# Performance work log

Hardware: AMD Instinct MI355X
Metric: run time of the kernel (lower is better)

The kernel has to match this reference:

```python
import jax, jax.numpy as jnp
import numpy as np

NUM_EMBEDDINGS = 8192
EMBEDDING_DIM = 256


def setup_inputs() -> dict:
    key = jax.random.key(0)
    k1, k2 = jax.random.split(key)
    z = jax.random.normal(k1, (16, EMBEDDING_DIM, 32, 32), dtype=jnp.float32)
    # nn.Embedding default init: N(0, 1)
    emb_table = jax.random.normal(k2, (NUM_EMBEDDINGS, EMBEDDING_DIM), dtype=jnp.float32)
    return {"z": z, "emb_table": emb_table}


def reference(z, emb_table):
    # z: [B, D, H, W]; emb_table: [K, D]
    B, D, H, W = z.shape
    # flatten to per-token vectors: [B*H*W, D]
    zf = z.reshape(B, D, H * W).transpose(0, 2, 1).reshape(B * H * W, D)
    Wt = jax.lax.stop_gradient(emb_table)  # original detaches W for distance
    # argmin of mean squared distance == argmin of squared distance;
    # expand ||z - w||^2 = ||z||^2 - 2 z.w + ||w||^2 (avoid (N,K,D) expansion)
    z_sq = jnp.sum(zf * zf, axis=-1, keepdims=True)          # [N, 1]
    w_sq = jnp.sum(Wt * Wt, axis=-1)                          # [K]
    dists = z_sq - 2.0 * (zf @ Wt.T) + w_sq                   # [N, K]
    token_ids = jnp.argmin(dists, axis=-1)                    # [N]
    quantized = emb_table[token_ids]                          # [N, D] (differentiable gather)
    return quantized.reshape(B, H * W, D).transpose(0, 2, 1).reshape(B, D, H, W)
```

## Files before the change

### kernel.cpp

```cpp
#include <hip/hip_runtime.h>
#include <stdint.h>

#define DIM 256
#define NEMB 8192
#define NTOK 16384
#define HW 1024

typedef __attribute__((ext_vector_type(4))) int int4v;

__device__ __forceinline__ void async_cp16(void* lds, const void* g) {
  __builtin_amdgcn_global_load_lds(
      (const __attribute__((address_space(1))) unsigned int*)g,
      (__attribute__((address_space(3))) unsigned int*)lds, 16, 0, 0);
}
__device__ __forceinline__ int q0_of(float x) {
  int q = __float2int_rn(x * 20.0f);
  return q > 127 ? 127 : (q < -127 ? -127 : q);
}
__device__ __forceinline__ int q1_of(float x, int q0) {
  float e = x * 20.0f - (float)q0;
  int q = __float2int_rn(e * 128.0f);
  return q > 127 ? 127 : (q < -127 ? -127 : q);
}
__device__ __forceinline__ unsigned int pack4(int a, int b, int c, int d) {
  return (unsigned int)(a & 0xff) | ((unsigned int)(b & 0xff) << 8) |
         ((unsigned int)(c & 0xff) << 16) | ((unsigned int)(d & 0xff) << 24);
}
__device__ __forceinline__ unsigned int med3u(unsigned int a, unsigned int b,
                                              unsigned int c) {
  unsigned int m;
  asm("v_med3_u32 %0, %1, %2, %3" : "=v"(m) : "v"(a), "v"(b), "v"(c));
  return m;
}
__device__ __forceinline__ void top3_insert(unsigned int v, unsigned int& m1,
                                            unsigned int& m2, unsigned int& m3) {
  unsigned int t2 = med3u(v, m1, m2);
  unsigned int t3 = med3u(v, m2, m3);
  m1 = v < m1 ? v : m1;
  m2 = t2;
  m3 = t3;
}

__global__ __launch_bounds__(256) void prep_kernel(
    const float* __restrict__ emb, unsigned int* __restrict__ q0w,
    unsigned int* __restrict__ q1w, int* __restrict__ iwsq2,
    const float* __restrict__ z, unsigned int* __restrict__ q0z) {
  __shared__ float tile[64][65];
  int tid = threadIdx.x;
  int lane = tid & 63;
  if (blockIdx.x < 2048) {
    int row = blockIdx.x * 4 + (tid >> 6);
    const float4 v = *(const float4*)(emb + (size_t)row * DIM + lane * 4);
    float s = v.x * v.x + v.y * v.y + v.z * v.z + v.w * v.w;
    int a0 = q0_of(v.x), b0 = q0_of(v.y), c0 = q0_of(v.z), d0 = q0_of(v.w);
    q0w[row * (DIM / 4) + lane] = pack4(a0, b0, c0, d0);
    q1w[row * (DIM / 4) + lane] =
        pack4(q1_of(v.x, a0), q1_of(v.y, b0), q1_of(v.z, c0), q1_of(v.w, d0));
#pragma unroll
    for (int off = 32; off > 0; off >>= 1) s += __shfl_xor(s, off, 64);
    if (lane == 0) iwsq2[row] = (int)rintf(s * 25600.0f) + 8192;
    return;
  }
  int idx = blockIdx.x - 2048;
  int b = idx >> 6, d0 = ((idx >> 4) & 3) * 64, hw0 = (idx & 15) * 64;
  int grp = tid >> 6;
  const float* src = z + (size_t)b * DIM * HW + hw0 + lane;
#pragma unroll
  for (int i = 0; i < 16; i++) {
    int dl = grp + i * 4;
    tile[dl][lane] = src[(size_t)(d0 + dl) * HW];
  }
  __syncthreads();
  int dq = tid & 15;
#pragma unroll
  for (int p = 0; p < 4; p++) {
    int n = (tid >> 4) + p * 16;
    int a0 = q0_of(tile[dq * 4 + 0][n]), b0 = q0_of(tile[dq * 4 + 1][n]);
    int c0 = q0_of(tile[dq * 4 + 2][n]), e0 = q0_of(tile[dq * 4 + 3][n]);
    int token = b * HW + hw0 + n;
    q0z[(size_t)token * (DIM / 4) + (d0 >> 2) + dq] = pack4(a0, b0, c0, e0);
  }
}

__global__ __launch_bounds__(512) void gemm_topk_kernel(
    const signed char* __restrict__ q0z, const signed char* __restrict__ q0w,
    const signed char* __restrict__ q1w, const int* __restrict__ iwsq2,
    uint4* __restrict__ partials) {
  __shared__ __align__(16) signed char sB[2][4][32 * 128];

  const int bid = blockIdx.x;
  const int kq = bid & 7;
  const int tg = bid >> 3;
  const int tid = threadIdx.x;
  const int lane = tid & 63, w = tid >> 6;
  const int c = lane & 15, quad = lane >> 4;
  const int n0 = tg * 256;
  const int k0g = kq * 1024;

  int4v af0[2][4];
#pragma unroll
  for (int t = 0; t < 2; t++) {
    const size_t arow = (size_t)(n0 + w * 32 + t * 16 + c) * DIM;
#pragma unroll
    for (int s = 0; s < 4; s++)
      af0[t][s] = *(const int4v*)(q0z + arow + s * 64 + quad * 16);
  }

  const int hi = tid >> 8;
  const int t2 = tid & 255;
  const int srow = t2 >> 3;
  const int scl = ((t2 & 7) ^ (srow & 7)) * 16;
  const signed char* p = (hi ? q1w : q0w) + (size_t)(k0g + srow) * DIM + scl;
  signed char* d0s = &sB[0][hi * 2][t2 * 16];
  signed char* d1s = &sB[0][hi * 2 + 1][t2 * 16];
  async_cp16(d0s, p);
  async_cp16(d1s, p + 128);
  p += 32 * DIM;
  __syncthreads();

  unsigned int m1[8], m2[8], m3[8];
#pragma unroll
  for (int i = 0; i < 8; i++) {
    m1[i] = 0xFFFFFFFFu; m2[i] = 0xFFFFFFFFu; m3[i] = 0xFFFFFFFFu;
  }

  unsigned int idxA = (unsigned)(k0g + c);
  const int4v zero = {0, 0, 0, 0};

  for (int it = 0; it < 32; it++) {
    const int buf = it & 1;
    if (it + 1 < 32) {
      const int nb = buf ^ 1;
      async_cp16(d0s + nb * 16384, p);
      async_cp16(d1s + nb * 16384, p + 128);
      p += 32 * DIM;
    }
    const int iw0 = iwsq2[k0g + it * 32 + c];
    const int iw1 = iwsq2[k0g + it * 32 + 16 + c];

    int4v a[2][2];
#pragma unroll
    for (int s = 0; s < 4; s++) {
      const int ph = ((((s & 1) << 2) + quad) ^ (c & 7)) * 16;
      int4v b0a = *(const int4v*)(&sB[buf][s >> 1][c * 128 + ph]);
      int4v b0b = *(const int4v*)(&sB[buf][s >> 1][(16 + c) * 128 + ph]);
      if (s == 0) {
#pragma unroll
        for (int t = 0; t < 2; t++) {
          a[t][0] = __builtin_amdgcn_mfma_i32_16x16x64_i8(af0[t][0], b0a, zero, 0, 0, 0);
          a[t][1] = __builtin_amdgcn_mfma_i32_16x16x64_i8(af0[t][0], b0b, zero, 0, 0, 0);
        }
      } else {
#pragma unroll
        for (int t = 0; t < 2; t++) {
          a[t][0] = __builtin_amdgcn_mfma_i32_16x16x64_i8(af0[t][s], b0a, a[t][0], 0, 0, 0);
          a[t][1] = __builtin_amdgcn_mfma_i32_16x16x64_i8(af0[t][s], b0b, a[t][1], 0, 0, 0);
        }
      }
    }
#pragma unroll
    for (int t = 0; t < 2; t++)
#pragma unroll
      for (int cn = 0; cn < 2; cn++)
#pragma unroll
        for (int r = 0; r < 4; r++) a[t][cn][r] <<= 7;
#pragma unroll
    for (int s = 0; s < 4; s++) {
      const int ph = ((((s & 1) << 2) + quad) ^ (c & 7)) * 16;
      int4v b1a = *(const int4v*)(&sB[buf][2 + (s >> 1)][c * 128 + ph]);
      int4v b1b = *(const int4v*)(&sB[buf][2 + (s >> 1)][(16 + c) * 128 + ph]);
#pragma unroll
      for (int t = 0; t < 2; t++) {
        a[t][0] = __builtin_amdgcn_mfma_i32_16x16x64_i8(af0[t][s], b1a, a[t][0], 0, 0, 0);
        a[t][1] = __builtin_amdgcn_mfma_i32_16x16x64_i8(af0[t][s], b1b, a[t][1], 0, 0, 0);
      }
    }
#pragma unroll
    for (int t = 0; t < 2; t++) {
#pragma unroll
      for (int r = 0; r < 4; r++) {
        unsigned int s0 = (unsigned int)(iw0 - a[t][0][r]);
        unsigned int s1 = (unsigned int)(iw1 - a[t][1][r]);
        unsigned int smin = s0 < s1 ? s0 : s1;
        unsigned int idx = s1 < s0 ? idxA + 16 : idxA;
        smin = smin < 0x1FFFFFFu ? smin : 0x1FFFFFFu;
        unsigned int pk = ((smin >> 6) << 13) | idx;
        top3_insert(pk, m1[t * 4 + r], m2[t * 4 + r], m3[t * 4 + r]);
      }
    }
    idxA += 32;
    __syncthreads();
  }

#pragma unroll
  for (int ix = 0; ix < 8; ix++) {
    unsigned int a1 = m1[ix], a2 = m2[ix], a3 = m3[ix];
#pragma unroll
    for (int off = 1; off < 16; off <<= 1) {
      unsigned int o1 = __shfl_xor(a1, off, 16);
      unsigned int o2 = __shfl_xor(a2, off, 16);
      unsigned int o3 = __shfl_xor(a3, off, 16);
      top3_insert(o1, a1, a2, a3);
      top3_insert(o2, a1, a2, a3);
      top3_insert(o3, a1, a2, a3);
    }
    m1[ix] = a1; m2[ix] = a2; m3[ix] = a3;
  }
  if (c == 0) {
#pragma unroll
    for (int t = 0; t < 2; t++) {
#pragma unroll
      for (int r = 0; r < 4; r++) {
        int token = n0 + w * 32 + t * 16 + quad * 4 + r;
        partials[(size_t)token * 8 + kq] =
            make_uint4(m1[t * 4 + r], m2[t * 4 + r], m3[t * 4 + r], 0xFFFFFFFFu);
      }
    }
  }
}

__global__ __launch_bounds__(256) void rescore_gather_kernel(
    const uint4* __restrict__ partials, const float* __restrict__ z,
    const float* __restrict__ emb, float* __restrict__ out) {
  __shared__ float tile[32][257];
  __shared__ int sid[32];
  __shared__ int wl[32];
  __shared__ int nwl;
  const int b = blockIdx.x >> 5;
  const int hw0 = (blockIdx.x & 31) * 32;
  const int tid = threadIdx.x;
  if (tid == 0) nwl = 0;
  __syncthreads();
  {
    const int tl = tid >> 3, sub = tid & 7;
    const int token = b * HW + hw0 + tl;
    uint4 e = partials[(size_t)token * 8 + sub];
    unsigned int m = e.x < e.y ? e.x : e.y;
    m = e.z < m ? e.z : m;
#pragma unroll
    for (int off = 1; off < 8; off <<= 1) {
      unsigned int o = __shfl_xor(m, off, 8);
      m = o < m ? o : m;
    }
    const unsigned int thr = (m >> 13) + 1536;
    int cnt = (((e.x >> 13) <= thr) ? 1 : 0) + (((e.y >> 13) <= thr) ? 1 : 0) +
              (((e.z >> 13) <= thr) ? 1 : 0);
#pragma unroll
    for (int off = 1; off < 8; off <<= 1) cnt += __shfl_xor(cnt, off, 8);
    if (sub == 0) {
      if (cnt == 1) {
        sid[tl] = (int)(m & 0x1FFFu);
      } else {
        int i = atomicAdd(&nwl, 1);
        wl[i] = tl;
      }
    }
  }
  __syncthreads();
  {
    const float* zp = z + (size_t)b * DIM * HW + (size_t)tid * HW + hw0;
#pragma unroll
    for (int h4 = 0; h4 < 8; h4++) {
      const float4 v = *(const float4*)(zp + h4 * 4);
      tile[h4 * 4 + 0][tid] = v.x;
      tile[h4 * 4 + 1][tid] = v.y;
      tile[h4 * 4 + 2][tid] = v.z;
      tile[h4 * 4 + 3][tid] = v.w;
    }
  }
  __syncthreads();
  {
    const int w = tid >> 6, lane = tid & 63;
    for (int i = w; i < nwl; i += 4) {
      const int tl = wl[i];
      const int token = b * HW + hw0 + tl;
      unsigned int p[24];
#pragma unroll
      for (int q = 0; q < 8; q++) {
        uint4 t = partials[(size_t)token * 8 + q];
        p[q * 3] = t.x;
        p[q * 3 + 1] = t.y;
        p[q * 3 + 2] = t.z;
      }
      unsigned int smin = p[0];
#pragma unroll
      for (int q = 1; q < 24; q++) smin = p[q] < smin ? p[q] : smin;
      const unsigned int thr = (smin >> 13) + 1536;
      float zv[4];
#pragma unroll
      for (int j = 0; j < 4; j++) zv[j] = tile[tl][lane * 4 + j];
      double best = 1e300;
      int bid2 = NEMB;
#pragma unroll
      for (int q = 0; q < 24; q++) {
        if ((p[q] >> 13) <= thr) {
          int id = (int)(p[q] & 0x1FFFu);
          const float4 wv = *(const float4*)(emb + (size_t)id * DIM + lane * 4);
          double s = (double)wv.x * ((double)wv.x - 2.0 * (double)zv[0]) +
                     (double)wv.y * ((double)wv.y - 2.0 * (double)zv[1]) +
                     (double)wv.z * ((double)wv.z - 2.0 * (double)zv[2]) +
                     (double)wv.w * ((double)wv.w - 2.0 * (double)zv[3]);
#pragma unroll
          for (int off = 32; off > 0; off >>= 1) s += __shfl_xor(s, off, 64);
          if (s < best || (s == best && id < bid2)) {
            best = s;
            bid2 = id;
          }
        }
      }
      if (lane == 0) sid[tl] = bid2;
    }
  }
  __syncthreads();
  for (int i = 0; i < 32; i++)
    tile[i][tid] = emb[(size_t)sid[i] * DIM + tid];
  __syncthreads();
  int h = tid & 31, dg = tid >> 5;
  for (int i = 0; i < 32; i++) {
    int d = i * 8 + dg;
    out[(size_t)b * DIM * HW + (size_t)d * HW + hw0 + h] = tile[h][d];
  }
}

extern "C" void kernel_launch(void* const* d_in, const int* in_sizes, int n_in,
                              void* d_out, int out_size, void* d_ws, size_t ws_size,
                              hipStream_t stream) {
  const float* z = (const float*)d_in[0];
  const float* emb = (const float*)d_in[1];
  float* out = (float*)d_out;
  char* ws = (char*)d_ws;

  signed char* q0w = (signed char*)(ws);
  signed char* q1w = (signed char*)(ws + 2097152);
  signed char* q0z = (signed char*)(ws + 4194304);
  int* iwsq2 = (int*)(ws + 8388608);
  uint4* partials = (uint4*)(ws + 8421376);

  prep_kernel<<<dim3(3072), 256, 0, stream>>>(
      emb, (unsigned int*)q0w, (unsigned int*)q1w, iwsq2, z, (unsigned int*)q0z);
  gemm_topk_kernel<<<dim3(512), 512, 0, stream>>>(q0z, q0w, q1w, iwsq2,
                                                  partials);
  rescore_gather_kernel<<<dim3(512), 256, 0, stream>>>(partials, z, emb, out);
}
```

Before: 158.0 us.

## Deepen B-tile prefetch to four LDS stages and halve barriers

The embedding-tile staging in LDS goes from a double buffer to a four-slot ring, loaded two iterations ahead. The loop is unrolled by four with compile-time buffer indices, and a barrier now follows every two iterations instead of every one. The aim is to hide more global-load latency and cut synchronisation overhead. The cost is twice the LDS per block (64 KB), which may reduce occupancy.

```diff
diff --git a/kernel.cpp b/kernel.cpp
--- a/kernel.cpp
+++ b/kernel.cpp
@@ -86,7 +86,7 @@
     const signed char* __restrict__ q0z, const signed char* __restrict__ q0w,
     const signed char* __restrict__ q1w, const int* __restrict__ iwsq2,
     uint4* __restrict__ partials) {
-  __shared__ __align__(16) signed char sB[2][4][32 * 128];
+  __shared__ __align__(16) signed char sB[4][4][32 * 128];
 
   const int bid = blockIdx.x;
   const int kq = bid & 7;
@@ -116,6 +116,9 @@
   async_cp16(d0s, p);
   async_cp16(d1s, p + 128);
   p += 32 * DIM;
+  async_cp16(d0s + 16384, p);
+  async_cp16(d1s + 16384, p + 128);
+  p += 32 * DIM;
   __syncthreads();
 
   unsigned int m1[8], m2[8], m3[8];
@@ -127,70 +130,69 @@
   unsigned int idxA = (unsigned)(k0g + c);
   const int4v zero = {0, 0, 0, 0};
 
-  for (int it = 0; it < 32; it++) {
-    const int buf = it & 1;
-    if (it + 1 < 32) {
-      const int nb = buf ^ 1;
-      async_cp16(d0s + nb * 16384, p);
-      async_cp16(d1s + nb * 16384, p + 128);
-      p += 32 * DIM;
-    }
-    const int iw0 = iwsq2[k0g + it * 32 + c];
-    const int iw1 = iwsq2[k0g + it * 32 + 16 + c];
-
-    int4v a[2][2];
-#pragma unroll
-    for (int s = 0; s < 4; s++) {
-      const int ph = ((((s & 1) << 2) + quad) ^ (c & 7)) * 16;
-      int4v b0a = *(const int4v*)(&sB[buf][s >> 1][c * 128 + ph]);
-      int4v b0b = *(const int4v*)(&sB[buf][s >> 1][(16 + c) * 128 + ph]);
-      if (s == 0) {
-#pragma unroll
-        for (int t = 0; t < 2; t++) {
-          a[t][0] = __builtin_amdgcn_mfma_i32_16x16x64_i8(af0[t][0], b0a, zero, 0, 0, 0);
-          a[t][1] = __builtin_amdgcn_mfma_i32_16x16x64_i8(af0[t][0], b0b, zero, 0, 0, 0);
-        }
-      } else {
-#pragma unroll
-        for (int t = 0; t < 2; t++) {
-          a[t][0] = __builtin_amdgcn_mfma_i32_16x16x64_i8(af0[t][s], b0a, a[t][0], 0, 0, 0);
-          a[t][1] = __builtin_amdgcn_mfma_i32_16x16x64_i8(af0[t][s], b0b, a[t][1], 0, 0, 0);
-        }
-      }
-    }
-#pragma unroll
-    for (int t = 0; t < 2; t++)
-#pragma unroll
-      for (int cn = 0; cn < 2; cn++)
-#pragma unroll
-        for (int r = 0; r < 4; r++) a[t][cn][r] <<= 7;
-#pragma unroll
-    for (int s = 0; s < 4; s++) {
-      const int ph = ((((s & 1) << 2) + quad) ^ (c & 7)) * 16;
-      int4v b1a = *(const int4v*)(&sB[buf][2 + (s >> 1)][c * 128 + ph]);
-      int4v b1b = *(const int4v*)(&sB[buf][2 + (s >> 1)][(16 + c) * 128 + ph]);
-#pragma unroll
-      for (int t = 0; t < 2; t++) {
-        a[t][0] = __builtin_amdgcn_mfma_i32_16x16x64_i8(af0[t][s], b1a, a[t][0], 0, 0, 0);
-        a[t][1] = __builtin_amdgcn_mfma_i32_16x16x64_i8(af0[t][s], b1b, a[t][1], 0, 0, 0);
-      }
-    }
-#pragma unroll
-    for (int t = 0; t < 2; t++) {
-#pragma unroll
-      for (int r = 0; r < 4; r++) {
-        unsigned int s0 = (unsigned int)(iw0 - a[t][0][r]);
-        unsigned int s1 = (unsigned int)(iw1 - a[t][1][r]);
-        unsigned int smin = s0 < s1 ? s0 : s1;
-        unsigned int idx = s1 < s0 ? idxA + 16 : idxA;
-        smin = smin < 0x1FFFFFFu ? smin : 0x1FFFFFFu;
-        unsigned int pk = ((smin >> 6) << 13) | idx;
-        top3_insert(pk, m1[t * 4 + r], m2[t * 4 + r], m3[t * 4 + r]);
-      }
-    }
-    idxA += 32;
+#define ITER(K, SB)                                                            \
+  {                                                                            \
+    const int it = i4 * 4 + (K);                                               \
+    if (it + 2 < 32) {                                                         \
+      async_cp16(d0s + (SB) * 16384, p);                                       \
+      async_cp16(d1s + (SB) * 16384, p + 128);                                 \
+      p += 32 * DIM;                                                           \
+    }                                                                          \
+    const int iw0 = iwsq2[k0g + it * 32 + c];                                  \
+    const int iw1 = iwsq2[k0g + it * 32 + 16 + c];                             \
+    int4v a[2][2];                                                             \
+    _Pragma("unroll") for (int s = 0; s < 4; s++) {                            \
+      const int ph = ((((s & 1) << 2) + quad) ^ (c & 7)) * 16;                 \
+      int4v b0a = *(const int4v*)(&sB[K][s >> 1][c * 128 + ph]);               \
+      int4v b0b = *(const int4v*)(&sB[K][s >> 1][(16 + c) * 128 + ph]);        \
+      if (s == 0) {                                                            \
+        _Pragma("unroll") for (int t = 0; t < 2; t++) {                        \
+          a[t][0] = __builtin_amdgcn_mfma_i32_16x16x64_i8(af0[t][0], b0a, zero, 0, 0, 0); \
+          a[t][1] = __builtin_amdgcn_mfma_i32_16x16x64_i8(af0[t][0], b0b, zero, 0, 0, 0); \
+        }                                                                      \
+      } else {                                                                 \
+        _Pragma("unroll") for (int t = 0; t < 2; t++) {                        \
+          a[t][0] = __builtin_amdgcn_mfma_i32_16x16x64_i8(af0[t][s], b0a, a[t][0], 0, 0, 0); \
+          a[t][1] = __builtin_amdgcn_mfma_i32_16x16x64_i8(af0[t][s], b0b, a[t][1], 0, 0, 0); \
+        }                                                                      \
+      }                                                                        \
+    }                                                                          \
+    _Pragma("unroll") for (int t = 0; t < 2; t++)                              \
+        _Pragma("unroll") for (int cn = 0; cn < 2; cn++)                       \
+        _Pragma("unroll") for (int r = 0; r < 4; r++) a[t][cn][r] <<= 7;       \
+    _Pragma("unroll") for (int s = 0; s < 4; s++) {                            \
+      const int ph = ((((s & 1) << 2) + quad) ^ (c & 7)) * 16;                 \
+      int4v b1a = *(const int4v*)(&sB[K][2 + (s >> 1)][c * 128 + ph]);         \
+      int4v b1b = *(const int4v*)(&sB[K][2 + (s >> 1)][(16 + c) * 128 + ph]);  \
+      _Pragma("unroll") for (int t = 0; t < 2; t++) {                          \
+        a[t][0] = __builtin_amdgcn_mfma_i32_16x16x64_i8(af0[t][s], b1a, a[t][0], 0, 0, 0); \
+        a[t][1] = __builtin_amdgcn_mfma_i32_16x16x64_i8(af0[t][s], b1b, a[t][1], 0, 0, 0); \
+      }                                                                        \
+    }                                                                          \
+    _Pragma("unroll") for (int t = 0; t < 2; t++) {                            \
+      _Pragma("unroll") for (int r = 0; r < 4; r++) {                          \
+        unsigned int s0 = (unsigned int)(iw0 - a[t][0][r]);                    \
+        unsigned int s1 = (unsigned int)(iw1 - a[t][1][r]);                    \
+        unsigned int smin = s0 < s1 ? s0 : s1;                                 \
+        unsigned int idx = s1 < s0 ? idxA + 16 : idxA;                         \
+        smin = smin < 0x1FFFFFFu ? smin : 0x1FFFFFFu;                          \
+        unsigned int pk = ((smin >> 6) << 13) | idx;                           \
+        top3_insert(pk, m1[t * 4 + r], m2[t * 4 + r], m3[t * 4 + r]);          \
+      }                                                                        \
+    }                                                                          \
+    idxA += 32;                                                                \
+  }
+
+#pragma unroll 1
+  for (int i4 = 0; i4 < 8; i4++) {
+    ITER(0, 2);
+    ITER(1, 3);
     __syncthreads();
-  }
+    ITER(2, 0);
+    ITER(3, 1);
+    __syncthreads();
+  }
+#undef ITER
 
 #pragma unroll
   for (int ix = 0; ix < 8; ix++) {
```

Result: no change. 157.3 us (-0.5%).

## Fuse prep, int8 GEMM top-k and rescore into one cooperative kernel

Applied to the files above, without the earlier changes.

Merges the three launches (quantization prep, int8 MFMA distance GEMM with top-3 selection, rescore and gather) into one cooperative kernel of 512 blocks, separated by grid-wide syncs. The intent is to remove two kernel launch gaps and the tail drain between stages. In exchange every stage is forced onto the same 512x512 grid and shared-memory footprint, and grid syncs add their own barrier cost. The old three-kernel path is kept as a fallback if the cooperative launch fails.

```diff
diff --git a/kernel.cpp b/kernel.cpp
--- a/kernel.cpp
+++ b/kernel.cpp
@@ -1,5 +1,8 @@
 #include <hip/hip_runtime.h>
+#include <hip/hip_cooperative_groups.h>
 #include <stdint.h>
+
+namespace cg = cooperative_groups;
 
 #define DIM 256
 #define NEMB 8192
@@ -39,6 +42,296 @@
   m1 = v < m1 ? v : m1;
   m2 = t2;
   m3 = t3;
+}
+
+__global__ __launch_bounds__(512) void fused_kernel(
+    const float* __restrict__ z, const float* __restrict__ emb,
+    float* __restrict__ out, signed char* __restrict__ q0w,
+    signed char* __restrict__ q1w, signed char* __restrict__ q0z,
+    int* __restrict__ iwsq2, uint4* __restrict__ partials) {
+  __shared__ __align__(16) unsigned char smem[33280];
+  __shared__ int sid[32];
+  __shared__ int wl[32];
+  __shared__ int nwl;
+
+  const int bid = blockIdx.x;
+  const int tid = threadIdx.x;
+  const int lane = tid & 63;
+  const int w = tid >> 6;
+
+#pragma unroll
+  for (int rr = 0; rr < 2; rr++) {
+    const int row = bid * 16 + w * 2 + rr;
+    const float4 v = *(const float4*)(emb + (size_t)row * DIM + lane * 4);
+    float s = v.x * v.x + v.y * v.y + v.z * v.z + v.w * v.w;
+    int a0 = q0_of(v.x), b0 = q0_of(v.y), c0 = q0_of(v.z), d0 = q0_of(v.w);
+    ((unsigned int*)q0w)[row * 64 + lane] = pack4(a0, b0, c0, d0);
+    ((unsigned int*)q1w)[row * 64 + lane] =
+        pack4(q1_of(v.x, a0), q1_of(v.y, b0), q1_of(v.z, c0), q1_of(v.w, d0));
+#pragma unroll
+    for (int off = 32; off > 0; off >>= 1) s += __shfl_xor(s, off, 64);
+    if (lane == 0) iwsq2[row] = (int)rintf(s * 25600.0f) + 8192;
+  }
+  {
+    float* zt = (float*)smem;
+    const int half = tid >> 8, t = tid & 255;
+    const int tl = t & 63, grp = t >> 6;
+    const int idx = bid * 2 + half;
+    const int b = idx >> 6, d0 = ((idx >> 4) & 3) * 64, hw0 = (idx & 15) * 64;
+    float* tz = zt + half * (64 * 65);
+    const float* src = z + (size_t)b * DIM * HW + hw0 + tl;
+#pragma unroll
+    for (int i = 0; i < 16; i++) {
+      int dl = grp + i * 4;
+      tz[dl * 65 + tl] = src[(size_t)(d0 + dl) * HW];
+    }
+    __syncthreads();
+    const int dq = t & 15;
+#pragma unroll
+    for (int p2 = 0; p2 < 4; p2++) {
+      int n = (t >> 4) + p2 * 16;
+      int a0 = q0_of(tz[(dq * 4 + 0) * 65 + n]);
+      int b0 = q0_of(tz[(dq * 4 + 1) * 65 + n]);
+      int c0 = q0_of(tz[(dq * 4 + 2) * 65 + n]);
+      int e0 = q0_of(tz[(dq * 4 + 3) * 65 + n]);
+      int token = b * HW + hw0 + n;
+      ((unsigned int*)q0z)[token * 64 + (d0 >> 2) + dq] = pack4(a0, b0, c0, e0);
+    }
+  }
+  cg::this_grid().sync();
+
+  {
+    signed char* sb = (signed char*)smem;
+    const int kq = bid & 7;
+    const int tg = bid >> 3;
+    const int c = lane & 15, quad = lane >> 4;
+    const int n0 = tg * 256;
+    const int k0g = kq * 1024;
+
+    int4v af0[2][4];
+#pragma unroll
+    for (int t = 0; t < 2; t++) {
+      const size_t arow = (size_t)(n0 + w * 32 + t * 16 + c) * DIM;
+#pragma unroll
+      for (int s = 0; s < 4; s++)
+        af0[t][s] = *(const int4v*)(q0z + arow + s * 64 + quad * 16);
+    }
+
+    const int hi = tid >> 8;
+    const int t2 = tid & 255;
+    const int srow = t2 >> 3;
+    const int scl = ((t2 & 7) ^ (srow & 7)) * 16;
+    const signed char* p = (hi ? q1w : q0w) + (size_t)(k0g + srow) * DIM + scl;
+    signed char* d0s = sb + hi * 2 * 4096 + t2 * 16;
+    signed char* d1s = d0s + 4096;
+    async_cp16(d0s, p);
+    async_cp16(d1s, p + 128);
+    p += 32 * DIM;
+    __syncthreads();
+
+    unsigned int m1[8], m2[8], m3[8];
+#pragma unroll
+    for (int i = 0; i < 8; i++) {
+      m1[i] = 0xFFFFFFFFu; m2[i] = 0xFFFFFFFFu; m3[i] = 0xFFFFFFFFu;
+    }
+    unsigned int idxA = (unsigned)(k0g + c);
+    const int4v zero = {0, 0, 0, 0};
+
+    for (int it = 0; it < 32; it++) {
+      const int buf = it & 1;
+      if (it + 1 < 32) {
+        const int nb = buf ^ 1;
+        async_cp16(d0s + nb * 16384, p);
+        async_cp16(d1s + nb * 16384, p + 128);
+        p += 32 * DIM;
+      }
+      const int iw0 = iwsq2[k0g + it * 32 + c];
+      const int iw1 = iwsq2[k0g + it * 32 + 16 + c];
+
+      int4v a[2][2];
+#pragma unroll
+      for (int s = 0; s < 4; s++) {
+        const int ph = ((((s & 1) << 2) + quad) ^ (c & 7)) * 16;
+        const signed char* base = sb + buf * 16384 + (s >> 1) * 4096;
+        int4v b0a = *(const int4v*)(base + c * 128 + ph);
+        int4v b0b = *(const int4v*)(base + (16 + c) * 128 + ph);
+        if (s == 0) {
+#pragma unroll
+          for (int t = 0; t < 2; t++) {
+            a[t][0] = __builtin_amdgcn_mfma_i32_16x16x64_i8(af0[t][0], b0a, zero, 0, 0, 0);
+            a[t][1] = __builtin_amdgcn_mfma_i32_16x16x64_i8(af0[t][0], b0b, zero, 0, 0, 0);
+          }
+        } else {
+#pragma unroll
+          for (int t = 0; t < 2; t++) {
+            a[t][0] = __builtin_amdgcn_mfma_i32_16x16x64_i8(af0[t][s], b0a, a[t][0], 0, 0, 0);
+            a[t][1] = __builtin_amdgcn_mfma_i32_16x16x64_i8(af0[t][s], b0b, a[t][1], 0, 0, 0);
+          }
+        }
+      }
+#pragma unroll
+      for (int t = 0; t < 2; t++)
+#pragma unroll
+        for (int cn = 0; cn < 2; cn++)
+#pragma unroll
+          for (int r = 0; r < 4; r++) a[t][cn][r] <<= 7;
+#pragma unroll
+      for (int s = 0; s < 4; s++) {
+        const int ph = ((((s & 1) << 2) + quad) ^ (c & 7)) * 16;
+        const signed char* base = sb + buf * 16384 + (2 + (s >> 1)) * 4096;
+        int4v b1a = *(const int4v*)(base + c * 128 + ph);
+        int4v b1b = *(const int4v*)(base + (16 + c) * 128 + ph);
+#pragma unroll
+        for (int t = 0; t < 2; t++) {
+          a[t][0] = __builtin_amdgcn_mfma_i32_16x16x64_i8(af0[t][s], b1a, a[t][0], 0, 0, 0);
+          a[t][1] = __builtin_amdgcn_mfma_i32_16x16x64_i8(af0[t][s], b1b, a[t][1], 0, 0, 0);
+        }
+      }
+#pragma unroll
+      for (int t = 0; t < 2; t++) {
+#pragma unroll
+        for (int r = 0; r < 4; r++) {
+          unsigned int s0 = (unsigned int)(iw0 - a[t][0][r]);
+          unsigned int s1 = (unsigned int)(iw1 - a[t][1][r]);
+          unsigned int smin = s0 < s1 ? s0 : s1;
+          unsigned int idx = s1 < s0 ? idxA + 16 : idxA;
+          smin = smin < 0x1FFFFFFu ? smin : 0x1FFFFFFu;
+          unsigned int pk = ((smin >> 6) << 13) | idx;
+          top3_insert(pk, m1[t * 4 + r], m2[t * 4 + r], m3[t * 4 + r]);
+        }
+      }
+      idxA += 32;
+      __syncthreads();
+    }
+
+#pragma unroll
+    for (int ix = 0; ix < 8; ix++) {
+      unsigned int a1 = m1[ix], a2 = m2[ix], a3 = m3[ix];
+#pragma unroll
+      for (int off = 1; off < 16; off <<= 1) {
+        unsigned int o1 = __shfl_xor(a1, off, 16);
+        unsigned int o2 = __shfl_xor(a2, off, 16);
+        unsigned int o3 = __shfl_xor(a3, off, 16);
+        top3_insert(o1, a1, a2, a3);
+        top3_insert(o2, a1, a2, a3);
+        top3_insert(o3, a1, a2, a3);
+      }
+      m1[ix] = a1; m2[ix] = a2; m3[ix] = a3;
+    }
+    if (c == 0) {
+#pragma unroll
+      for (int t = 0; t < 2; t++) {
+#pragma unroll
+        for (int r = 0; r < 4; r++) {
+          int token = n0 + w * 32 + t * 16 + quad * 4 + r;
+          partials[(size_t)token * 8 + kq] =
+              make_uint4(m1[t * 4 + r], m2[t * 4 + r], m3[t * 4 + r], 0xFFFFFFFFu);
+        }
+      }
+    }
+  }
+  cg::this_grid().sync();
+
+  {
+    float* tile = (float*)smem;
+    const int b = bid >> 5;
+    const int hw0 = (bid & 31) * 32;
+    if (tid == 0) nwl = 0;
+    __syncthreads();
+    if (tid < 256) {
+      const int tl = tid >> 3, sub = tid & 7;
+      const int token = b * HW + hw0 + tl;
+      uint4 e = partials[(size_t)token * 8 + sub];
+      unsigned int m = e.x < e.y ? e.x : e.y;
+      m = e.z < m ? e.z : m;
+#pragma unroll
+      for (int off = 1; off < 8; off <<= 1) {
+        unsigned int o = __shfl_xor(m, off, 8);
+        m = o < m ? o : m;
+      }
+      const unsigned int thr = (m >> 13) + 1536;
+      int cnt = (((e.x >> 13) <= thr) ? 1 : 0) + (((e.y >> 13) <= thr) ? 1 : 0) +
+                (((e.z >> 13) <= thr) ? 1 : 0);
+#pragma unroll
+      for (int off = 1; off < 8; off <<= 1) cnt += __shfl_xor(cnt, off, 8);
+      if (sub == 0) {
+        if (cnt == 1) {
+          sid[tl] = (int)(m & 0x1FFFu);
+        } else {
+          int i = atomicAdd(&nwl, 1);
+          wl[i] = tl;
+        }
+      }
+    }
+    __syncthreads();
+    if (tid < 256) {
+      const float* zp = z + (size_t)b * DIM * HW + (size_t)tid * HW + hw0;
+#pragma unroll
+      for (int h4 = 0; h4 < 8; h4++) {
+        const float4 v = *(const float4*)(zp + h4 * 4);
+        tile[(h4 * 4 + 0) * 257 + tid] = v.x;
+        tile[(h4 * 4 + 1) * 257 + tid] = v.y;
+        tile[(h4 * 4 + 2) * 257 + tid] = v.z;
+        tile[(h4 * 4 + 3) * 257 + tid] = v.w;
+      }
+    }
+    __syncthreads();
+    {
+      const int w8 = tid >> 6;
+      for (int i = w8; i < nwl; i += 8) {
+        const int tl = wl[i];
+        const int token = b * HW + hw0 + tl;
+        unsigned int pq[24];
+#pragma unroll
+        for (int q = 0; q < 8; q++) {
+          uint4 t = partials[(size_t)token * 8 + q];
+          pq[q * 3] = t.x;
+          pq[q * 3 + 1] = t.y;
+          pq[q * 3 + 2] = t.z;
+        }
+        unsigned int smin = pq[0];
+#pragma unroll
+        for (int q = 1; q < 24; q++) smin = pq[q] < smin ? pq[q] : smin;
+        const unsigned int thr = (smin >> 13) + 1536;
+        float zv[4];
+#pragma unroll
+        for (int j = 0; j < 4; j++) zv[j] = tile[tl * 257 + lane * 4 + j];
+        double best = 1e300;
+        int bid2 = NEMB;
+#pragma unroll
+        for (int q = 0; q < 24; q++) {
+          if ((pq[q] >> 13) <= thr) {
+            int id = (int)(pq[q] & 0x1FFFu);
+            const float4 wv = *(const float4*)(emb + (size_t)id * DIM + lane * 4);
+            double s = (double)wv.x * ((double)wv.x - 2.0 * (double)zv[0]) +
+                       (double)wv.y * ((double)wv.y - 2.0 * (double)zv[1]) +
+                       (double)wv.z * ((double)wv.z - 2.0 * (double)zv[2]) +
+                       (double)wv.w * ((double)wv.w - 2.0 * (double)zv[3]);
+#pragma unroll
+            for (int off = 32; off > 0; off >>= 1) s += __shfl_xor(s, off, 64);
+            if (s < best || (s == best && id < bid2)) {
+              best = s;
+              bid2 = id;
+            }
+          }
+        }
+        if (lane == 0) sid[tl] = bid2;
+      }
+    }
+    __syncthreads();
+    for (int i = 0; i < 16; i++) {
+      int row = i * 2 + (tid >> 8);
+      tile[row * 257 + (tid & 255)] = emb[(size_t)sid[row] * DIM + (tid & 255)];
+    }
+    __syncthreads();
+    {
+      const int h = tid & 31, dg = tid >> 5;
+      for (int i = 0; i < 16; i++) {
+        int d = i * 16 + dg;
+        out[(size_t)b * DIM * HW + (size_t)d * HW + hw0 + h] = tile[h * 257 + d];
+      }
+    }
+  }
 }
 
 __global__ __launch_bounds__(256) void prep_kernel(
@@ -87,7 +380,6 @@
     const signed char* __restrict__ q1w, const int* __restrict__ iwsq2,
     uint4* __restrict__ partials) {
   __shared__ __align__(16) signed char sB[2][4][32 * 128];
-
   const int bid = blockIdx.x;
   const int kq = bid & 7;
   const int tg = bid >> 3;
@@ -96,7 +388,6 @@
   const int c = lane & 15, quad = lane >> 4;
   const int n0 = tg * 256;
   const int k0g = kq * 1024;
-
   int4v af0[2][4];
 #pragma unroll
   for (int t = 0; t < 2; t++) {
@@ -105,7 +396,6 @@
     for (int s = 0; s < 4; s++)
       af0[t][s] = *(const int4v*)(q0z + arow + s * 64 + quad * 16);
   }
-
   const int hi = tid >> 8;
   const int t2 = tid & 255;
   const int srow = t2 >> 3;
@@ -117,16 +407,13 @@
   async_cp16(d1s, p + 128);
   p += 32 * DIM;
   __syncthreads();
-
   unsigned int m1[8], m2[8], m3[8];
 #pragma unroll
   for (int i = 0; i < 8; i++) {
     m1[i] = 0xFFFFFFFFu; m2[i] = 0xFFFFFFFFu; m3[i] = 0xFFFFFFFFu;
   }
-
   unsigned int idxA = (unsigned)(k0g + c);
   const int4v zero = {0, 0, 0, 0};
-
   for (int it = 0; it < 32; it++) {
     const int buf = it & 1;
     if (it + 1 < 32) {
@@ -137,7 +424,6 @@
     }
     const int iw0 = iwsq2[k0g + it * 32 + c];
     const int iw1 = iwsq2[k0g + it * 32 + 16 + c];
-
     int4v a[2][2];
 #pragma unroll
     for (int s = 0; s < 4; s++) {
@@ -191,7 +477,6 @@
     idxA += 32;
     __syncthreads();
   }
-
 #pragma unroll
   for (int ix = 0; ix < 8; ix++) {
     unsigned int a1 = m1[ix], a2 = m2[ix], a3 = m3[ix];
@@ -336,9 +621,23 @@
   int* iwsq2 = (int*)(ws + 8388608);
   uint4* partials = (uint4*)(ws + 8421376);
 
-  prep_kernel<<<dim3(3072), 256, 0, stream>>>(
-      emb, (unsigned int*)q0w, (unsigned int*)q1w, iwsq2, z, (unsigned int*)q0z);
-  gemm_topk_kernel<<<dim3(512), 512, 0, stream>>>(q0z, q0w, q1w, iwsq2,
-                                                  partials);
-  rescore_gather_kernel<<<dim3(512), 256, 0, stream>>>(partials, z, emb, out);
-}
+  void* args[8];
+  args[0] = (void*)&z;
+  args[1] = (void*)&emb;
+  args[2] = (void*)&out;
+  args[3] = (void*)&q0w;
+  args[4] = (void*)&q1w;
+  args[5] = (void*)&q0z;
+  args[6] = (void*)&iwsq2;
+  args[7] = (void*)&partials;
+  hipError_t err = hipLaunchCooperativeKernel(
+      (const void*)fused_kernel, dim3(512), dim3(512), args, 0, stream);
+  if (err != hipSuccess) {
+    prep_kernel<<<dim3(3072), 256, 0, stream>>>(
+        emb, (unsigned int*)q0w, (unsigned int*)q1w, iwsq2, z,
+        (unsigned int*)q0z);
+    gemm_topk_kernel<<<dim3(512), 512, 0, stream>>>(q0z, q0w, q1w, iwsq2,
+                                                    partials);
+    rescore_gather_kernel<<<dim3(512), 256, 0, stream>>>(partials, z, emb, out);
+  }
+}
```

New measurement: 261.2 us. 65.3% more time.
